# Optimization experiments

Measured on AMD Instinct MI355X. Metric: run time of the kernel, lower is better.

Reference implementation:

```python
import jax, jax.numpy as jnp
import numpy as np
from jax import lax

B, T = 16384, 1000


def setup_inputs() -> dict:
    key = jax.random.key(0)
    k1, k2, k3, k4 = jax.random.split(key, 4)
    xicovs = jax.random.normal(k1, (B, T, 2, 2), dtype=jnp.float32) * 0.1
    dy = jax.random.normal(k2, (B, T, 2), dtype=jnp.float32) * 0.1
    coeffs_A = jax.random.normal(k3, (2, 2), dtype=jnp.float32) * 0.05
    C = jax.random.normal(k4, (2, 2), dtype=jnp.float32)
    x0 = jnp.zeros((B, 2), dtype=jnp.float32)
    dt = jnp.ones((1,), dtype=jnp.float32) * 0.001
    return {"xicovs": xicovs, "dy": dy, "coeffs_A": coeffs_A, "C": C, "x0": x0, "dt": dt}


def reference(xicovs, dy, coeffs_A, C, x0, dt):
    """Unrolls the GaussianDynamics recurrent cell over T steps with lax.scan.

    Per step (faithful to the original call):
      A_m  = coeffs_A - xicov @ C                     # [B,2,2]
      out  = (C @ x_prev) * dt                        # emitted output
      x    = x_prev + (A_m @ x_prev) * dt + xicov @ dy_t
    Returns (outputs [B,T,2], final_state [B,2]).
    """
    dts = dt[0]

    def step(x, inp):
        xic, dyt = inp  # [B,2,2], [B,2]
        A_m = coeffs_A - jnp.einsum('bij,jk->bik', xic, C)
        out = jnp.einsum('ij,bj->bi', C, x) * dts
        x_new = x + jnp.einsum('bij,bj->bi', A_m, x) * dts + jnp.einsum('bij,bj->bi', xic, dyt)
        return x_new, out

    xs = (jnp.moveaxis(xicovs, 1, 0), jnp.moveaxis(dy, 1, 0))  # time-major
    x_final, outs = lax.scan(step, x0, xs)
    return jnp.moveaxis(outs, 0, 1), x_final
```

## Files before the change

### kernel.cpp

```cpp
#include <hip/hip_runtime.h>


constexpr int BATCH = 16384;
constexpr int TLEN  = 1000;
constexpr int TPB   = 256;
constexpr int SPT   = 4;
constexpr int TPAD  = 1024;

typedef float vfloat4 __attribute__((ext_vector_type(4)));
typedef float vfloat2 __attribute__((ext_vector_type(2)));

__global__ __launch_bounds__(TPB, 6) void gd_scan_kernel(
    const float* __restrict__ xicovs,
    const float* __restrict__ dyv,
    const float* __restrict__ cA,
    const float* __restrict__ Cm,
    const float* __restrict__ x0,
    const float* __restrict__ dtp,
    float* __restrict__ out)
{
    __shared__ float s_xi00[TPAD], s_xi01[TPAD], s_xi10[TPAD], s_xi11[TPAD];
    __shared__ float s_dy0[TPAD], s_dy1[TPAD];
    __shared__ float wsum[TPB / 64][6];

    const int b    = blockIdx.x;
    const int tid  = threadIdx.x;
    const int lane = tid & 63;
    const int wv   = tid >> 6;

    {
        const vfloat4* gx = reinterpret_cast<const vfloat4*>(xicovs + (size_t)b * TLEN * 4);
        for (int i = tid; i < TLEN; i += TPB) {
            const vfloat4 v = gx[i];
            s_xi00[i] = v.x; s_xi01[i] = v.y; s_xi10[i] = v.z; s_xi11[i] = v.w;
        }
        const vfloat2* gd = reinterpret_cast<const vfloat2*>(dyv + (size_t)b * TLEN * 2);
        for (int i = tid; i < TLEN; i += TPB) {
            const vfloat2 v = gd[i];
            s_dy0[i] = v.x; s_dy1[i] = v.y;
        }
    }

    const float dts = dtp[0];
    const float C00 = Cm[0], C01 = Cm[1], C10 = Cm[2], C11 = Cm[3];
    const float A00 = cA[0], A01 = cA[1], A10 = cA[2], A11 = cA[3];

    __syncthreads();

    const int t0 = tid * SPT;

    const vfloat4 q00 = *reinterpret_cast<const vfloat4*>(&s_xi00[t0]);
    const vfloat4 q01 = *reinterpret_cast<const vfloat4*>(&s_xi01[t0]);
    const vfloat4 q10 = *reinterpret_cast<const vfloat4*>(&s_xi10[t0]);
    const vfloat4 q11 = *reinterpret_cast<const vfloat4*>(&s_xi11[t0]);
    const vfloat4 qd0 = *reinterpret_cast<const vfloat4*>(&s_dy0[t0]);
    const vfloat4 qd1 = *reinterpret_cast<const vfloat4*>(&s_dy1[t0]);

    const float xi00s[SPT] = {q00.x, q00.y, q00.z, q00.w};
    const float xi01s[SPT] = {q01.x, q01.y, q01.z, q01.w};
    const float xi10s[SPT] = {q10.x, q10.y, q10.z, q10.w};
    const float xi11s[SPT] = {q11.x, q11.y, q11.z, q11.w};
    const float dy0s[SPT]  = {qd0.x, qd0.y, qd0.z, qd0.w};
    const float dy1s[SPT]  = {qd1.x, qd1.y, qd1.z, qd1.w};

    float S00s[SPT], S01s[SPT], S10s[SPT], S11s[SPT], o0s[SPT], o1s[SPT];
    float M00 = 1.f, M01 = 0.f, M10 = 0.f, M11 = 1.f, c0 = 0.f, c1 = 0.f;
#pragma unroll
    for (int s = 0; s < SPT; ++s) {
        const int t = t0 + s;
        const float xi00 = xi00s[s], xi01 = xi01s[s], xi10 = xi10s[s], xi11 = xi11s[s];
        const float Am00 = A00 - (xi00 * C00 + xi01 * C10);
        const float Am01 = A01 - (xi00 * C01 + xi01 * C11);
        const float Am10 = A10 - (xi10 * C00 + xi11 * C10);
        const float Am11 = A11 - (xi10 * C01 + xi11 * C11);
        float S00 = 1.f + Am00 * dts, S01 = Am01 * dts;
        float S10 = Am10 * dts,       S11 = 1.f + Am11 * dts;
        float o0 = xi00 * dy0s[s] + xi01 * dy1s[s];
        float o1 = xi10 * dy0s[s] + xi11 * dy1s[s];
        if (t >= TLEN) { S00 = 1.f; S01 = 0.f; S10 = 0.f; S11 = 1.f; o0 = 0.f; o1 = 0.f; }
        S00s[s] = S00; S01s[s] = S01; S10s[s] = S10; S11s[s] = S11; o0s[s] = o0; o1s[s] = o1;
        const float n00 = S00 * M00 + S01 * M10;
        const float n01 = S00 * M01 + S01 * M11;
        const float n10 = S10 * M00 + S11 * M10;
        const float n11 = S10 * M01 + S11 * M11;
        const float nc0 = S00 * c0 + S01 * c1 + o0;
        const float nc1 = S10 * c0 + S11 * c1 + o1;
        M00 = n00; M01 = n01; M10 = n10; M11 = n11; c0 = nc0; c1 = nc1;
    }

#pragma unroll
    for (int off = 1; off < 64; off <<= 1) {
        const float m00 = __shfl_up(M00, off);
        const float m01 = __shfl_up(M01, off);
        const float m10 = __shfl_up(M10, off);
        const float m11 = __shfl_up(M11, off);
        const float lc0 = __shfl_up(c0,  off);
        const float lc1 = __shfl_up(c1,  off);
        if (lane >= off) {
            const float n00 = M00 * m00 + M01 * m10;
            const float n01 = M00 * m01 + M01 * m11;
            const float n10 = M10 * m00 + M11 * m10;
            const float n11 = M10 * m01 + M11 * m11;
            const float nc0 = M00 * lc0 + M01 * lc1 + c0;
            const float nc1 = M10 * lc0 + M11 * lc1 + c1;
            M00 = n00; M01 = n01; M10 = n10; M11 = n11; c0 = nc0; c1 = nc1;
        }
    }

    if (lane == 63) {
        wsum[wv][0] = M00; wsum[wv][1] = M01; wsum[wv][2] = M10; wsum[wv][3] = M11;
        wsum[wv][4] = c0;  wsum[wv][5] = c1;
    }
    __syncthreads();

    float P00 = 1.f, P01 = 0.f, P10 = 0.f, P11 = 1.f, Pc0 = 0.f, Pc1 = 0.f;
    for (int w = 0; w < wv; ++w) {
        const float w00 = wsum[w][0], w01 = wsum[w][1], w10 = wsum[w][2], w11 = wsum[w][3];
        const float wc0 = wsum[w][4], wc1 = wsum[w][5];
        const float n00 = w00 * P00 + w01 * P10;
        const float n01 = w00 * P01 + w01 * P11;
        const float n10 = w10 * P00 + w11 * P10;
        const float n11 = w10 * P01 + w11 * P11;
        const float nc0 = w00 * Pc0 + w01 * Pc1 + wc0;
        const float nc1 = w10 * Pc0 + w11 * Pc1 + wc1;
        P00 = n00; P01 = n01; P10 = n10; P11 = n11; Pc0 = nc0; Pc1 = nc1;
    }

    float e00 = __shfl_up(M00, 1), e01 = __shfl_up(M01, 1);
    float e10 = __shfl_up(M10, 1), e11 = __shfl_up(M11, 1);
    float ec0 = __shfl_up(c0, 1),  ec1 = __shfl_up(c1, 1);
    if (lane == 0) { e00 = 1.f; e01 = 0.f; e10 = 0.f; e11 = 1.f; ec0 = 0.f; ec1 = 0.f; }

    const float E00 = e00 * P00 + e01 * P10;
    const float E01 = e00 * P01 + e01 * P11;
    const float E10 = e10 * P00 + e11 * P10;
    const float E11 = e10 * P01 + e11 * P11;
    const float Ec0 = e00 * Pc0 + e01 * Pc1 + ec0;
    const float Ec1 = e10 * Pc0 + e11 * Pc1 + ec1;

    const float xa = x0[2 * b], xb = x0[2 * b + 1];
    float xq0 = E00 * xa + E01 * xb + Ec0;
    float xq1 = E10 * xa + E11 * xb + Ec1;

    float o0v[SPT], o1v[SPT];
#pragma unroll
    for (int s = 0; s < SPT; ++s) {
        o0v[s] = (C00 * xq0 + C01 * xq1) * dts;
        o1v[s] = (C10 * xq0 + C11 * xq1) * dts;
        const float nx0 = S00s[s] * xq0 + S01s[s] * xq1 + o0s[s];
        const float nx1 = S10s[s] * xq0 + S11s[s] * xq1 + o1s[s];
        xq0 = nx0; xq1 = nx1;
    }

    float* ob = out + (size_t)b * TLEN * 2 + (size_t)t0 * 2;
    if (t0 + SPT <= TLEN) {
        vfloat4 w0 = {o0v[0], o1v[0], o0v[1], o1v[1]};
        vfloat4 w1 = {o0v[2], o1v[2], o0v[3], o1v[3]};
        __builtin_nontemporal_store(w0, reinterpret_cast<vfloat4*>(ob));
        __builtin_nontemporal_store(w1, reinterpret_cast<vfloat4*>(ob) + 1);
    } else {
        for (int s = 0; s < SPT; ++s)
            if (t0 + s < TLEN) {
                vfloat2 w = {o0v[s], o1v[s]};
                __builtin_nontemporal_store(w, reinterpret_cast<vfloat2*>(ob) + s);
            }
    }

    if (t0 < TLEN && t0 + SPT >= TLEN) {
        float* xf = out + (size_t)BATCH * TLEN * 2 + 2 * b;
        xf[0] = xq0; xf[1] = xq1;
    }
}

extern "C" void kernel_launch(void* const* d_in, const int* in_sizes, int n_in,
                              void* d_out, int out_size, void* d_ws, size_t ws_size,
                              hipStream_t stream) {
    const float* xicovs = (const float*)d_in[0];
    const float* dyv    = (const float*)d_in[1];
    const float* cA     = (const float*)d_in[2];
    const float* Cm     = (const float*)d_in[3];
    const float* x0     = (const float*)d_in[4];
    const float* dtp    = (const float*)d_in[5];
    float* out = (float*)d_out;

    gd_scan_kernel<<<BATCH, TPB, 0, stream>>>(xicovs, dyv, cA, Cm, x0, dtp, out);
}
```

Before: 108.5 us.

## Process eight batch rows per block with register prefetch of next row

Each block now handles eight consecutive batch rows instead of one, and the grid shrinks to match. While the current row is staged in shared memory and scanned, the next row's xicov and dy values are loaded into registers so the global loads overlap the scan compute and barriers. The launch-bounds occupancy hint is lowered from 6 to 4 to leave room for the prefetch registers. The aim is to hide load latency and cut per-block launch and setup cost. The trade-off is fewer resident waves and more serialised work per block, on a kernel that is already close to memory-bandwidth bound.

```diff
diff --git a/kernel.cpp b/kernel.cpp
--- a/kernel.cpp
+++ b/kernel.cpp
@@ -5,12 +5,13 @@
 constexpr int TLEN  = 1000;
 constexpr int TPB   = 256;
 constexpr int SPT   = 4;
-constexpr int TPAD  = 1024;
+constexpr int ROWS  = 8;
+constexpr int NBLK  = BATCH / ROWS;
 
 typedef float vfloat4 __attribute__((ext_vector_type(4)));
 typedef float vfloat2 __attribute__((ext_vector_type(2)));
 
-__global__ __launch_bounds__(TPB, 6) void gd_scan_kernel(
+__global__ __launch_bounds__(TPB, 4) void gd_scan_kernel(
     const float* __restrict__ xicovs,
     const float* __restrict__ dyv,
     const float* __restrict__ cA,
@@ -19,156 +20,183 @@
     const float* __restrict__ dtp,
     float* __restrict__ out)
 {
-    __shared__ float s_xi00[TPAD], s_xi01[TPAD], s_xi10[TPAD], s_xi11[TPAD];
-    __shared__ float s_dy0[TPAD], s_dy1[TPAD];
+    __shared__ float s_xi00[TLEN], s_xi01[TLEN], s_xi10[TLEN], s_xi11[TLEN];
+    __shared__ float s_dy0[TLEN],  s_dy1[TLEN];
     __shared__ float wsum[TPB / 64][6];
 
-    const int b    = blockIdx.x;
     const int tid  = threadIdx.x;
     const int lane = tid & 63;
     const int wv   = tid >> 6;
-
-    {
-        const vfloat4* gx = reinterpret_cast<const vfloat4*>(xicovs + (size_t)b * TLEN * 4);
-        for (int i = tid; i < TLEN; i += TPB) {
-            const vfloat4 v = gx[i];
-            s_xi00[i] = v.x; s_xi01[i] = v.y; s_xi10[i] = v.z; s_xi11[i] = v.w;
-        }
-        const vfloat2* gd = reinterpret_cast<const vfloat2*>(dyv + (size_t)b * TLEN * 2);
-        for (int i = tid; i < TLEN; i += TPB) {
-            const vfloat2 v = gd[i];
-            s_dy0[i] = v.x; s_dy1[i] = v.y;
-        }
-    }
+    const int row0 = blockIdx.x * ROWS;
 
     const float dts = dtp[0];
     const float C00 = Cm[0], C01 = Cm[1], C10 = Cm[2], C11 = Cm[3];
     const float A00 = cA[0], A01 = cA[1], A10 = cA[2], A11 = cA[3];
 
-    __syncthreads();
-
-    const int t0 = tid * SPT;
-
-    const vfloat4 q00 = *reinterpret_cast<const vfloat4*>(&s_xi00[t0]);
-    const vfloat4 q01 = *reinterpret_cast<const vfloat4*>(&s_xi01[t0]);
-    const vfloat4 q10 = *reinterpret_cast<const vfloat4*>(&s_xi10[t0]);
-    const vfloat4 q11 = *reinterpret_cast<const vfloat4*>(&s_xi11[t0]);
-    const vfloat4 qd0 = *reinterpret_cast<const vfloat4*>(&s_dy0[t0]);
-    const vfloat4 qd1 = *reinterpret_cast<const vfloat4*>(&s_dy1[t0]);
-
-    const float xi00s[SPT] = {q00.x, q00.y, q00.z, q00.w};
-    const float xi01s[SPT] = {q01.x, q01.y, q01.z, q01.w};
-    const float xi10s[SPT] = {q10.x, q10.y, q10.z, q10.w};
-    const float xi11s[SPT] = {q11.x, q11.y, q11.z, q11.w};
-    const float dy0s[SPT]  = {qd0.x, qd0.y, qd0.z, qd0.w};
-    const float dy1s[SPT]  = {qd1.x, qd1.y, qd1.z, qd1.w};
-
-    float S00s[SPT], S01s[SPT], S10s[SPT], S11s[SPT], o0s[SPT], o1s[SPT];
-    float M00 = 1.f, M01 = 0.f, M10 = 0.f, M11 = 1.f, c0 = 0.f, c1 = 0.f;
-#pragma unroll
-    for (int s = 0; s < SPT; ++s) {
-        const int t = t0 + s;
-        const float xi00 = xi00s[s], xi01 = xi01s[s], xi10 = xi10s[s], xi11 = xi11s[s];
-        const float Am00 = A00 - (xi00 * C00 + xi01 * C10);
-        const float Am01 = A01 - (xi00 * C01 + xi01 * C11);
-        const float Am10 = A10 - (xi10 * C00 + xi11 * C10);
-        const float Am11 = A11 - (xi10 * C01 + xi11 * C11);
-        float S00 = 1.f + Am00 * dts, S01 = Am01 * dts;
-        float S10 = Am10 * dts,       S11 = 1.f + Am11 * dts;
-        float o0 = xi00 * dy0s[s] + xi01 * dy1s[s];
-        float o1 = xi10 * dy0s[s] + xi11 * dy1s[s];
-        if (t >= TLEN) { S00 = 1.f; S01 = 0.f; S10 = 0.f; S11 = 1.f; o0 = 0.f; o1 = 0.f; }
-        S00s[s] = S00; S01s[s] = S01; S10s[s] = S10; S11s[s] = S11; o0s[s] = o0; o1s[s] = o1;
-        const float n00 = S00 * M00 + S01 * M10;
-        const float n01 = S00 * M01 + S01 * M11;
-        const float n10 = S10 * M00 + S11 * M10;
-        const float n11 = S10 * M01 + S11 * M11;
-        const float nc0 = S00 * c0 + S01 * c1 + o0;
-        const float nc1 = S10 * c0 + S11 * c1 + o1;
-        M00 = n00; M01 = n01; M10 = n10; M11 = n11; c0 = nc0; c1 = nc1;
+    const int t0  = tid * SPT;
+    const int t0m = (t0 <= TLEN - SPT) ? t0 : (TLEN - SPT);
+
+    vfloat4 pf_x[4];
+    vfloat2 pf_d[4];
+
+    {
+        const vfloat4* gx = reinterpret_cast<const vfloat4*>(xicovs + (size_t)row0 * TLEN * 4);
+        const vfloat2* gd = reinterpret_cast<const vfloat2*>(dyv    + (size_t)row0 * TLEN * 2);
+#pragma unroll
+        for (int k = 0; k < 4; ++k) {
+            int i = tid + k * TPB; if (i >= TLEN) i = TLEN - 1;
+            pf_x[k] = gx[i];
+            pf_d[k] = gd[i];
+        }
     }
 
-#pragma unroll
-    for (int off = 1; off < 64; off <<= 1) {
-        const float m00 = __shfl_up(M00, off);
-        const float m01 = __shfl_up(M01, off);
-        const float m10 = __shfl_up(M10, off);
-        const float m11 = __shfl_up(M11, off);
-        const float lc0 = __shfl_up(c0,  off);
-        const float lc1 = __shfl_up(c1,  off);
-        if (lane >= off) {
-            const float n00 = M00 * m00 + M01 * m10;
-            const float n01 = M00 * m01 + M01 * m11;
-            const float n10 = M10 * m00 + M11 * m10;
-            const float n11 = M10 * m01 + M11 * m11;
-            const float nc0 = M00 * lc0 + M01 * lc1 + c0;
-            const float nc1 = M10 * lc0 + M11 * lc1 + c1;
+    for (int r = 0; r < ROWS; ++r) {
+        const int row = row0 + r;
+
+#pragma unroll
+        for (int k = 0; k < 4; ++k) {
+            const int i = tid + k * TPB;
+            if (i < TLEN) {
+                s_xi00[i] = pf_x[k].x; s_xi01[i] = pf_x[k].y;
+                s_xi10[i] = pf_x[k].z; s_xi11[i] = pf_x[k].w;
+                s_dy0[i]  = pf_d[k].x; s_dy1[i]  = pf_d[k].y;
+            }
+        }
+
+        if (r + 1 < ROWS) {
+            const vfloat4* gx = reinterpret_cast<const vfloat4*>(xicovs + (size_t)(row + 1) * TLEN * 4);
+            const vfloat2* gd = reinterpret_cast<const vfloat2*>(dyv    + (size_t)(row + 1) * TLEN * 2);
+#pragma unroll
+            for (int k = 0; k < 4; ++k) {
+                int i = tid + k * TPB; if (i >= TLEN) i = TLEN - 1;
+                pf_x[k] = gx[i];
+                pf_d[k] = gd[i];
+            }
+        }
+
+        __syncthreads();
+
+        const vfloat4 q00 = *reinterpret_cast<const vfloat4*>(&s_xi00[t0m]);
+        const vfloat4 q01 = *reinterpret_cast<const vfloat4*>(&s_xi01[t0m]);
+        const vfloat4 q10 = *reinterpret_cast<const vfloat4*>(&s_xi10[t0m]);
+        const vfloat4 q11 = *reinterpret_cast<const vfloat4*>(&s_xi11[t0m]);
+        const vfloat4 qd0 = *reinterpret_cast<const vfloat4*>(&s_dy0[t0m]);
+        const vfloat4 qd1 = *reinterpret_cast<const vfloat4*>(&s_dy1[t0m]);
+
+        const float xi00s[SPT] = {q00.x, q00.y, q00.z, q00.w};
+        const float xi01s[SPT] = {q01.x, q01.y, q01.z, q01.w};
+        const float xi10s[SPT] = {q10.x, q10.y, q10.z, q10.w};
+        const float xi11s[SPT] = {q11.x, q11.y, q11.z, q11.w};
+        const float dy0s[SPT]  = {qd0.x, qd0.y, qd0.z, qd0.w};
+        const float dy1s[SPT]  = {qd1.x, qd1.y, qd1.z, qd1.w};
+
+        float S00s[SPT], S01s[SPT], S10s[SPT], S11s[SPT], o0s[SPT], o1s[SPT];
+        float M00 = 1.f, M01 = 0.f, M10 = 0.f, M11 = 1.f, c0 = 0.f, c1 = 0.f;
+#pragma unroll
+        for (int s = 0; s < SPT; ++s) {
+            const int t = t0 + s;
+            const float xi00 = xi00s[s], xi01 = xi01s[s], xi10 = xi10s[s], xi11 = xi11s[s];
+            const float Am00 = A00 - (xi00 * C00 + xi01 * C10);
+            const float Am01 = A01 - (xi00 * C01 + xi01 * C11);
+            const float Am10 = A10 - (xi10 * C00 + xi11 * C10);
+            const float Am11 = A11 - (xi10 * C01 + xi11 * C11);
+            float S00 = 1.f + Am00 * dts, S01 = Am01 * dts;
+            float S10 = Am10 * dts,       S11 = 1.f + Am11 * dts;
+            float o0 = xi00 * dy0s[s] + xi01 * dy1s[s];
+            float o1 = xi10 * dy0s[s] + xi11 * dy1s[s];
+            if (t >= TLEN) { S00 = 1.f; S01 = 0.f; S10 = 0.f; S11 = 1.f; o0 = 0.f; o1 = 0.f; }
+            S00s[s] = S00; S01s[s] = S01; S10s[s] = S10; S11s[s] = S11; o0s[s] = o0; o1s[s] = o1;
+            const float n00 = S00 * M00 + S01 * M10;
+            const float n01 = S00 * M01 + S01 * M11;
+            const float n10 = S10 * M00 + S11 * M10;
+            const float n11 = S10 * M01 + S11 * M11;
+            const float nc0 = S00 * c0 + S01 * c1 + o0;
+            const float nc1 = S10 * c0 + S11 * c1 + o1;
             M00 = n00; M01 = n01; M10 = n10; M11 = n11; c0 = nc0; c1 = nc1;
         }
-    }
-
-    if (lane == 63) {
-        wsum[wv][0] = M00; wsum[wv][1] = M01; wsum[wv][2] = M10; wsum[wv][3] = M11;
-        wsum[wv][4] = c0;  wsum[wv][5] = c1;
-    }
-    __syncthreads();
-
-    float P00 = 1.f, P01 = 0.f, P10 = 0.f, P11 = 1.f, Pc0 = 0.f, Pc1 = 0.f;
-    for (int w = 0; w < wv; ++w) {
-        const float w00 = wsum[w][0], w01 = wsum[w][1], w10 = wsum[w][2], w11 = wsum[w][3];
-        const float wc0 = wsum[w][4], wc1 = wsum[w][5];
-        const float n00 = w00 * P00 + w01 * P10;
-        const float n01 = w00 * P01 + w01 * P11;
-        const float n10 = w10 * P00 + w11 * P10;
-        const float n11 = w10 * P01 + w11 * P11;
-        const float nc0 = w00 * Pc0 + w01 * Pc1 + wc0;
-        const float nc1 = w10 * Pc0 + w11 * Pc1 + wc1;
-        P00 = n00; P01 = n01; P10 = n10; P11 = n11; Pc0 = nc0; Pc1 = nc1;
-    }
-
-    float e00 = __shfl_up(M00, 1), e01 = __shfl_up(M01, 1);
-    float e10 = __shfl_up(M10, 1), e11 = __shfl_up(M11, 1);
-    float ec0 = __shfl_up(c0, 1),  ec1 = __shfl_up(c1, 1);
-    if (lane == 0) { e00 = 1.f; e01 = 0.f; e10 = 0.f; e11 = 1.f; ec0 = 0.f; ec1 = 0.f; }
-
-    const float E00 = e00 * P00 + e01 * P10;
-    const float E01 = e00 * P01 + e01 * P11;
-    const float E10 = e10 * P00 + e11 * P10;
-    const float E11 = e10 * P01 + e11 * P11;
-    const float Ec0 = e00 * Pc0 + e01 * Pc1 + ec0;
-    const float Ec1 = e10 * Pc0 + e11 * Pc1 + ec1;
-
-    const float xa = x0[2 * b], xb = x0[2 * b + 1];
-    float xq0 = E00 * xa + E01 * xb + Ec0;
-    float xq1 = E10 * xa + E11 * xb + Ec1;
-
-    float o0v[SPT], o1v[SPT];
-#pragma unroll
-    for (int s = 0; s < SPT; ++s) {
-        o0v[s] = (C00 * xq0 + C01 * xq1) * dts;
-        o1v[s] = (C10 * xq0 + C11 * xq1) * dts;
-        const float nx0 = S00s[s] * xq0 + S01s[s] * xq1 + o0s[s];
-        const float nx1 = S10s[s] * xq0 + S11s[s] * xq1 + o1s[s];
-        xq0 = nx0; xq1 = nx1;
-    }
-
-    float* ob = out + (size_t)b * TLEN * 2 + (size_t)t0 * 2;
-    if (t0 + SPT <= TLEN) {
-        vfloat4 w0 = {o0v[0], o1v[0], o0v[1], o1v[1]};
-        vfloat4 w1 = {o0v[2], o1v[2], o0v[3], o1v[3]};
-        __builtin_nontemporal_store(w0, reinterpret_cast<vfloat4*>(ob));
-        __builtin_nontemporal_store(w1, reinterpret_cast<vfloat4*>(ob) + 1);
-    } else {
-        for (int s = 0; s < SPT; ++s)
-            if (t0 + s < TLEN) {
-                vfloat2 w = {o0v[s], o1v[s]};
-                __builtin_nontemporal_store(w, reinterpret_cast<vfloat2*>(ob) + s);
+
+#pragma unroll
+        for (int off = 1; off < 64; off <<= 1) {
+            const float m00 = __shfl_up(M00, off);
+            const float m01 = __shfl_up(M01, off);
+            const float m10 = __shfl_up(M10, off);
+            const float m11 = __shfl_up(M11, off);
+            const float lc0 = __shfl_up(c0,  off);
+            const float lc1 = __shfl_up(c1,  off);
+            if (lane >= off) {
+                const float n00 = M00 * m00 + M01 * m10;
+                const float n01 = M00 * m01 + M01 * m11;
+                const float n10 = M10 * m00 + M11 * m10;
+                const float n11 = M10 * m01 + M11 * m11;
+                const float nc0 = M00 * lc0 + M01 * lc1 + c0;
+                const float nc1 = M10 * lc0 + M11 * lc1 + c1;
+                M00 = n00; M01 = n01; M10 = n10; M11 = n11; c0 = nc0; c1 = nc1;
             }
-    }
-
-    if (t0 < TLEN && t0 + SPT >= TLEN) {
-        float* xf = out + (size_t)BATCH * TLEN * 2 + 2 * b;
-        xf[0] = xq0; xf[1] = xq1;
+        }
+
+        if (lane == 63) {
+            wsum[wv][0] = M00; wsum[wv][1] = M01; wsum[wv][2] = M10; wsum[wv][3] = M11;
+            wsum[wv][4] = c0;  wsum[wv][5] = c1;
+        }
+        __syncthreads();
+
+        float P00 = 1.f, P01 = 0.f, P10 = 0.f, P11 = 1.f, Pc0 = 0.f, Pc1 = 0.f;
+        for (int w = 0; w < wv; ++w) {
+            const float w00 = wsum[w][0], w01 = wsum[w][1], w10 = wsum[w][2], w11 = wsum[w][3];
+            const float wc0 = wsum[w][4], wc1 = wsum[w][5];
+            const float n00 = w00 * P00 + w01 * P10;
+            const float n01 = w00 * P01 + w01 * P11;
+            const float n10 = w10 * P00 + w11 * P10;
+            const float n11 = w10 * P01 + w11 * P11;
+            const float nc0 = w00 * Pc0 + w01 * Pc1 + wc0;
+            const float nc1 = w10 * Pc0 + w11 * Pc1 + wc1;
+            P00 = n00; P01 = n01; P10 = n10; P11 = n11; Pc0 = nc0; Pc1 = nc1;
+        }
+
+        float e00 = __shfl_up(M00, 1), e01 = __shfl_up(M01, 1);
+        float e10 = __shfl_up(M10, 1), e11 = __shfl_up(M11, 1);
+        float ec0 = __shfl_up(c0, 1),  ec1 = __shfl_up(c1, 1);
+        if (lane == 0) { e00 = 1.f; e01 = 0.f; e10 = 0.f; e11 = 1.f; ec0 = 0.f; ec1 = 0.f; }
+
+        const float E00 = e00 * P00 + e01 * P10;
+        const float E01 = e00 * P01 + e01 * P11;
+        const float E10 = e10 * P00 + e11 * P10;
+        const float E11 = e10 * P01 + e11 * P11;
+        const float Ec0 = e00 * Pc0 + e01 * Pc1 + ec0;
+        const float Ec1 = e10 * Pc0 + e11 * Pc1 + ec1;
+
+        const float xa = x0[2 * row], xb = x0[2 * row + 1];
+        float xq0 = E00 * xa + E01 * xb + Ec0;
+        float xq1 = E10 * xa + E11 * xb + Ec1;
+
+        float o0v[SPT], o1v[SPT];
+#pragma unroll
+        for (int s = 0; s < SPT; ++s) {
+            o0v[s] = (C00 * xq0 + C01 * xq1) * dts;
+            o1v[s] = (C10 * xq0 + C11 * xq1) * dts;
+            const float nx0 = S00s[s] * xq0 + S01s[s] * xq1 + o0s[s];
+            const float nx1 = S10s[s] * xq0 + S11s[s] * xq1 + o1s[s];
+            xq0 = nx0; xq1 = nx1;
+        }
+
+        float* ob = out + (size_t)row * TLEN * 2 + (size_t)t0 * 2;
+        if (t0 + SPT <= TLEN) {
+            vfloat4 w0 = {o0v[0], o1v[0], o0v[1], o1v[1]};
+            vfloat4 w1 = {o0v[2], o1v[2], o0v[3], o1v[3]};
+            __builtin_nontemporal_store(w0, reinterpret_cast<vfloat4*>(ob));
+            __builtin_nontemporal_store(w1, reinterpret_cast<vfloat4*>(ob) + 1);
+        } else {
+            for (int s = 0; s < SPT; ++s)
+                if (t0 + s < TLEN) {
+                    vfloat2 w = {o0v[s], o1v[s]};
+                    __builtin_nontemporal_store(w, reinterpret_cast<vfloat2*>(ob) + s);
+                }
+        }
+
+        if (t0 < TLEN && t0 + SPT >= TLEN) {
+            float* xf = out + (size_t)BATCH * TLEN * 2 + 2 * row;
+            xf[0] = xq0; xf[1] = xq1;
+        }
     }
 }
 
@@ -183,5 +211,5 @@
     const float* dtp    = (const float*)d_in[5];
     float* out = (float*)d_out;
 
-    gd_scan_kernel<<<BATCH, TPB, 0, stream>>>(xicovs, dyv, cA, Cm, x0, dtp, out);
+    gd_scan_kernel<<<NBLK, TPB, 0, stream>>>(xicovs, dyv, cA, Cm, x0, dtp, out);
 }
```

After: 130.6 us. 20.4% more time.
